# Performance work log

Measured on AMD Instinct MI355X. Metric: run time of the kernel, lower is better.

The kernel has to match this reference:

```python
import jax, jax.numpy as jnp
import numpy as np

N, CIN, PL, H, W, ETA, EXP = 8, 1024, 256, 64, 64, 8, 4
EPS = 1e-5

def _conv(x, w, stride=1, pad=0):
    return jax.lax.conv_general_dilated(
        x, w, (stride, stride), [(pad, pad), (pad, pad)],
        dimension_numbers=('NCHW', 'OIHW', 'NCHW'))

def _bn(x, p):
    # p: [4, C] = gamma, beta, running_mean, running_var (eval-mode BN)
    g, b, m, v = p[0], p[1], p[2], p[3]
    scale = (g / jnp.sqrt(v + EPS))[None, :, None, None]
    return (x - m[None, :, None, None]) * scale + b[None, :, None, None]

def _bn_params(key, c):
    k1, k2, k3, k4 = jax.random.split(key, 4)
    return jnp.stack([
        1.0 + 0.1 * jax.random.normal(k1, (c,)),
        0.1 * jax.random.normal(k2, (c,)),
        0.1 * jax.random.normal(k3, (c,)),
        jax.random.uniform(k4, (c,), minval=0.5, maxval=1.5)]).astype(jnp.float32)

def setup_inputs() -> dict:
    key = jax.random.key(0)
    ks = jax.random.split(key, 12)
    return {
        'x': jax.random.normal(ks[0], (N, CIN, H, W), jnp.float32),
        'norm_1': jnp.zeros((1, N + 1), jnp.float32),
        'norm_2': jnp.zeros((1, N + 1), jnp.float32),
        'flops': jnp.zeros((1, N + 1), jnp.float32),
        'ws_conv': 0.02 * jax.random.normal(ks[1], (1, CIN, 3, 3), jnp.float32),
        'ws_bias': jnp.zeros((1,), jnp.float32),
        'wc1': 0.02 * jax.random.normal(ks[2], (PL, CIN), jnp.float32),
        'bc1': jnp.zeros((PL,), jnp.float32),
        'wc2': 0.02 * jax.random.normal(ks[3], (PL, PL), jnp.float32),
        'bc2': jnp.zeros((PL,), jnp.float32),
        'w1': 0.05 * jax.random.normal(ks[4], (PL, CIN, 1, 1), jnp.float32),
        'bn1': _bn_params(ks[5], PL),
        'w2': 0.02 * jax.random.normal(ks[6], (PL, PL, 3, 3), jnp.float32),
        'bn2': _bn_params(ks[7], PL),
        'w3': 0.05 * jax.random.normal(ks[8], (PL * EXP, PL, 1, 1), jnp.float32),
        'bn3': _bn_params(ks[9], PL * EXP),
    }

def reference(x, norm_1, norm_2, flops, ws_conv, ws_bias, wc1, bc1, wc2, bc2,
              w1, bn1, w2, bn2, w3, bn3):
    n, c, h1, w1s = x.shape
    dt = x.dtype
    # ---- Mask_s: avg-pool by eta -> 3x3 conv to 1 ch -> hard gate (eval) ----
    pooled = x.reshape(n, c, h1 // ETA, ETA, w1s // ETA, ETA).mean((3, 5))
    logit_s = _conv(pooled, ws_conv, pad=1) + ws_bias[None, :, None, None]
    mask_s_m = (logit_s >= 0).astype(dt)            # [n,1,h/eta,w/eta]
    norm_s = mask_s_m.sum((1, 2, 3))                # [n]
    # ---- Mask_c1: GAP -> FC -> hard gate -> [n,PL,1,1] ----
    vec1 = x.mean((2, 3))                            # [n,CIN]
    mc1 = ((vec1 @ wc1.T + bc1) >= 0).astype(dt)[:, :, None, None]
    norm_c1 = mc1.sum((1, 2, 3))
    norm_c1_t = jnp.array([PL], dt)
    # ---- main path ----
    out = jax.nn.relu(_bn(_conv(x, w1), bn1))
    # nearest upsample of spatial mask back to (h1, w1)
    mask_s1 = jnp.repeat(jnp.repeat(mask_s_m, ETA, axis=2), ETA, axis=3)
    out = out * mc1 * mask_s1                        # eval-mode: both masks applied
    # ---- Mask_c2 on gated features ----
    vec2 = out.mean((2, 3))
    mc2 = ((vec2 @ wc2.T + bc2) >= 0).astype(dt)[:, :, None, None]
    norm_c2 = mc2.sum((1, 2, 3))
    norm_c2_t = jnp.array([PL], dt)
    out = jax.nn.relu(_bn(_conv(out, w2, pad=1), bn2))
    h2, w2s = out.shape[2], out.shape[3]
    mask_s2 = mask_s1                                # stride=1 -> same spatial size
    out = out * mc2 * mask_s2
    out = _bn(_conv(out, w3), bn3) * mask_s2
    out = jax.nn.relu(out + x)                       # identity (downsample=None)
    # ---- bookkeeping ----
    numel_s = jnp.array([mask_s_m[0].size], dt)      # 1 * h/eta * w/eta
    norm_1 = jnp.concatenate([norm_1, jnp.concatenate([norm_s, numel_s])[None]], 0)
    norm_2 = jnp.concatenate([norm_2, jnp.concatenate([norm_c1, norm_c1_t])[None]], 0)
    norm_2 = jnp.concatenate([norm_2, jnp.concatenate([norm_c2, norm_c2_t])[None]], 0)
    s_sum = mask_s2.sum((1, 2, 3))
    s_sum_1 = mask_s1.sum((1, 2, 3))
    fl = (s_sum_1 * norm_c1 * CIN
          + 9.0 * s_sum * norm_c2 * norm_c1
          + s_sum * (PL * EXP) * norm_c2)
    fl_full = jnp.array([h1 * w1s * PL * CIN
                         + 9 * h2 * w2s * PL * PL
                         + h2 * w2s * PL * PL * EXP], dt)
    flops = jnp.concatenate([flops, jnp.concatenate([fl, fl_full])[None]], 0)
    return out, norm_1, norm_2, flops
```

## Files before the change

### kernel.cpp

```cpp
#include <hip/hip_runtime.h>
#include <cstddef>
#include <cstdint>

#define NN   8
#define CIN  1024
#define PL   256
#define PE   1024
#define HW   4096
#define EPS_ 1e-5f

typedef _Float16 half8 __attribute__((ext_vector_type(8)));
typedef float floatx4 __attribute__((ext_vector_type(4)));

union HU { uint4 u4; half8 h8; };

__device__ inline uint32_t pack2(float v) {
  union { _Float16 f[2]; uint32_t u; } z;
  _Float16 h = (_Float16)v;
  z.f[0] = h;
  z.f[1] = (_Float16)(v - (float)h);
  return z.u;
}

static const size_t OFF1 = 33554432;
static const size_t OFF2 = OFF1 + 18;
static const size_t OFF3 = OFF2 + 27;

__global__ __launch_bounds__(256) void k_prep(
    const float* __restrict__ bn1, const float* __restrict__ bn2,
    const float* __restrict__ bn3, const float* __restrict__ w1,
    const float* __restrict__ w2, const float* __restrict__ w3,
    _Float16* __restrict__ w1f, _Float16* __restrict__ w2f,
    _Float16* __restrict__ w3f,
    float* __restrict__ s1, float* __restrict__ t1,
    float* __restrict__ s2, float* __restrict__ t2,
    float* __restrict__ s3, float* __restrict__ t3,
    float* __restrict__ pooled, float* __restrict__ vec2) {
  unsigned idx = blockIdx.x * 256 + threadIdx.x;
  if (idx < 262144u) {
    int p = idx >> 10, c = idx & 1023;
    float v = w1[idx]; _Float16 h = (_Float16)v;
    int lane = (((c & 31) >> 3) << 4) | (p & 15);
    size_t base = (size_t)(((c >> 5) * 16 + (p >> 4))) * 1024 + lane * 8 + (c & 7);
    w1f[base] = h; w1f[base + 512] = (_Float16)(v - (float)h);
  } else if (idx < 524288u) {
    unsigned i = idx - 262144u;
    int p = i >> 8, c = i & 255;
    float v = w3[i]; _Float16 h = (_Float16)v;
    int lane = (((c & 31) >> 3) << 4) | (p & 15);
    size_t base = (size_t)((c >> 5) * 64 + (p >> 4)) * 1024 + lane * 8 + (c & 7);
    w3f[base] = h; w3f[base + 512] = (_Float16)(v - (float)h);
  } else if (idx < 1114112u) {
    unsigned i = idx - 524288u;
    unsigned p = i / 2304u, rem = i - p * 2304u;
    unsigned c = rem / 9u, tap = rem - c * 9u;
    float v = w2[i]; _Float16 h = (_Float16)v;
    int lane = (((c & 31) >> 3) << 4) | (p & 15);
    size_t base = (size_t)((tap * 8 + (c >> 5)) * 16 + (p >> 4)) * 1024 + lane * 8 + (c & 7);
    w2f[base] = h; w2f[base + 512] = (_Float16)(v - (float)h);
  } else if (idx < 1638400u) {
    pooled[idx - 1114112u] = 0.f;
  } else if (idx < 1640448u) {
    vec2[idx - 1638400u] = 0.f;
  } else if (idx < 1641984u) {
    int i = idx - 1640448u;
    if (i < 256) {
      float g = bn1[i], b = bn1[256 + i], m = bn1[512 + i], v = bn1[768 + i];
      float s = g / sqrtf(v + EPS_);
      s1[i] = s; t1[i] = b - m * s;
    } else if (i < 512) {
      int c = i - 256;
      float g = bn2[c], b = bn2[256 + c], m = bn2[512 + c], v = bn2[768 + c];
      float s = g / sqrtf(v + EPS_);
      s2[c] = s; t2[c] = b - m * s;
    } else {
      int c = i - 512;
      float g = bn3[c], b = bn3[1024 + c], m = bn3[2048 + c], v = bn3[3072 + c];
      float s = g / sqrtf(v + EPS_);
      s3[c] = s; t3[c] = b - m * s;
    }
  }
}

__global__ __launch_bounds__(256) void k_xsplit(const float* __restrict__ x,
                                                _Float16* __restrict__ xh,
                                                _Float16* __restrict__ xl,
                                                float* __restrict__ pooled) {
  const int bx = blockIdx.x;
  const int hw0 = bx * 64, c0 = blockIdx.y * 64, n = blockIdx.z;
  const int t = threadIdx.x;
  __shared__ float Tt[64][65];
#pragma unroll
  for (int j = 0; j < 4; ++j) {
    int rc = (t >> 4) + j * 16;
    int col = (t & 15) * 4;
    float4 v = *(const float4*)(x + ((size_t)(n * 1024) + c0 + rc) * 4096 + hw0 + col);
    Tt[col + 0][rc] = v.x; Tt[col + 1][rc] = v.y;
    Tt[col + 2][rc] = v.z; Tt[col + 3][rc] = v.w;
  }
  __syncthreads();
  {
    const int ch = t & 63, grp = t >> 6;
    const int pr = bx >> 3;
#pragma unroll
    for (int cc = 0; cc < 2; ++cc) {
      int pc = grp * 2 + cc;
      float s = 0.f;
#pragma unroll
      for (int px = 0; px < 8; ++px) s += Tt[pc * 8 + px][ch];
      atomicAdd(&pooled[(size_t)(n * 64 + pr * 8 + pc) * 1024 + c0 + ch], s * (1.f / 64.f));
    }
  }
  const int hwl = t >> 2, part = t & 3;
  size_t ob = ((size_t)(n * 4096) + hw0 + hwl) * 1024 + c0 + part * 16;
#pragma unroll
  for (int k2 = 0; k2 < 2; ++k2) {
    half8 vh, vl;
#pragma unroll
    for (int e = 0; e < 8; ++e) {
      float v = Tt[hwl][part * 16 + k2 * 8 + e];
      _Float16 hh = (_Float16)v;
      vh[e] = hh; vl[e] = (_Float16)(v - (float)hh);
    }
    *(half8*)(xh + ob + k2 * 8) = vh;
    *(half8*)(xl + ob + k2 * 8) = vl;
  }
}

__global__ __launch_bounds__(256) void k_vec1(const float* __restrict__ pooled,
                                              float* __restrict__ vec1) {
  const int n = blockIdx.x, t = threadIdx.x;
#pragma unroll
  for (int j = 0; j < 4; ++j) {
    int c = j * 256 + t;
    float s = 0.f;
    for (int cell = 0; cell < 64; ++cell)
      s += pooled[(size_t)(n * 64 + cell) * 1024 + c];
    vec1[n * 1024 + c] = s * (1.f / 64.f);
  }
}

__global__ __launch_bounds__(256) void k_masks(const float* __restrict__ wsconv,
                                               const float* __restrict__ wsbias,
                                               const float* __restrict__ pooled,
                                               float* __restrict__ masks) {
  const int bid = blockIdx.x;
  const int n = bid >> 6, cell = bid & 63, ph = cell >> 3, pw = cell & 7;
  const int tid = threadIdx.x;
  const float* pl = pooled + (size_t)n * 64 * 1024;
  float acc = 0.f;
#pragma unroll
  for (int kh = 0; kh < 3; ++kh) {
    int py = ph + kh - 1;
    if (py < 0 || py > 7) continue;
#pragma unroll
    for (int kw = 0; kw < 3; ++kw) {
      int px = pw + kw - 1;
      if (px < 0 || px > 7) continue;
      float4 pv = *(const float4*)(pl + (size_t)(py * 8 + px) * 1024 + tid * 4);
      int k = kh * 3 + kw;
      acc += pv.x * wsconv[(tid * 4 + 0) * 9 + k] + pv.y * wsconv[(tid * 4 + 1) * 9 + k]
           + pv.z * wsconv[(tid * 4 + 2) * 9 + k] + pv.w * wsconv[(tid * 4 + 3) * 9 + k];
    }
  }
  __shared__ float red[256];
  red[tid] = acc;
  __syncthreads();
  for (int s = 128; s > 0; s >>= 1) {
    if (tid < s) red[tid] += red[tid + s];
    __syncthreads();
  }
  if (tid == 0) masks[n * 64 + cell] = (red[0] + wsbias[0] >= 0.f) ? 1.f : 0.f;
}

__global__ __launch_bounds__(64) void k_mc1(const float* __restrict__ wc1,
                                            const float* __restrict__ bc1,
                                            const float* __restrict__ vec1,
                                            float* __restrict__ mc1) {
  const int bx = blockIdx.x;
  const int n = bx >> 8, p = bx & 255;
  const int t = threadIdx.x;
  const float* v = vec1 + n * 1024;
  const float* wr = wc1 + (size_t)p * 1024;
  float acc = 0.f;
#pragma unroll
  for (int j = 0; j < 16; ++j) acc += v[t + 64 * j] * wr[t + 64 * j];
  for (int m = 1; m < 64; m <<= 1) acc += __shfl_xor(acc, m, 64);
  if (t == 0) mc1[n * 256 + p] = (acc + bc1[p] >= 0.f) ? 1.f : 0.f;
}

__global__ __launch_bounds__(256) void k_gemm1(
    const _Float16* __restrict__ xh, const _Float16* __restrict__ xl,
    const _Float16* __restrict__ w1f,
    const float* __restrict__ s1, const float* __restrict__ t1,
    const float* __restrict__ mc1, const float* __restrict__ masks,
    _Float16* __restrict__ o1h, _Float16* __restrict__ o1l) {
  const int hw0 = blockIdx.x * 128, p0 = blockIdx.y * 128, n = blockIdx.z;
  const int t = threadIdx.x;
  const int lane = t & 63, w = t >> 6;
  const int l15 = lane & 15, l4 = lane >> 4;
  const int wr = w >> 1, wc = w & 1;
  __shared__ __align__(16) char smem[33792];
  _Float16* LB = (_Float16*)smem;
  floatx4 acc[4][4] = {};
  const size_t nb = (size_t)(n * 4096) + hw0;
  const _Float16* wfp = w1f + (size_t)((p0 >> 4) + wr * 4) * 1024 + lane * 8;
  for (int kc = 0; kc < 32; ++kc) {
    const int c0 = kc * 32;
    half8 tmp[4];
#pragma unroll
    for (int j = 0; j < 4; ++j) {
      int u = t + 256 * j;
      int kind = u >> 9, rem = u & 511, row = rem >> 2, q = rem & 3;
      const _Float16* src = (kind ? xl : xh) + (nb + row) * 1024 + c0 + q * 8;
      tmp[j] = *(const half8*)src;
    }
    half8 ah[4], al[4];
#pragma unroll
    for (int i = 0; i < 4; ++i) {
      const _Float16* ap = wfp + (size_t)(kc * 16 + i) * 1024;
      ah[i] = *(const half8*)ap;
      al[i] = *(const half8*)(ap + 512);
    }
    __syncthreads();
#pragma unroll
    for (int j = 0; j < 4; ++j) {
      int u = t + 256 * j;
      int kind = u >> 9, rem = u & 511, row = rem >> 2, q = rem & 3;
      *(half8*)(LB + kind * 5120 + row * 40 + q * 8) = tmp[j];
    }
    __syncthreads();
    half8 bh[4], bl[4];
#pragma unroll
    for (int j = 0; j < 4; ++j) {
      int r = (wc * 64 + j * 16 + l15) * 40 + l4 * 8;
      bh[j] = *(const half8*)(LB + r);
      bl[j] = *(const half8*)(LB + 5120 + r);
    }
#pragma unroll
    for (int i = 0; i < 4; ++i)
#pragma unroll
      for (int j = 0; j < 4; ++j) {
        acc[i][j] = __builtin_amdgcn_mfma_f32_16x16x32_f16(ah[i], bh[j], acc[i][j], 0, 0, 0);
        acc[i][j] = __builtin_amdgcn_mfma_f32_16x16x32_f16(ah[i], bl[j], acc[i][j], 0, 0, 0);
        acc[i][j] = __builtin_amdgcn_mfma_f32_16x16x32_f16(al[i], bh[j], acc[i][j], 0, 0, 0);
      }
  }
  uint32_t (*T)[132] = (uint32_t(*)[132])smem;
  const int n64 = n * 64;
  const float* mc1n = mc1 + n * 256;
  for (int h = 0; h < 2; ++h) {
    __syncthreads();
    if (wc == h) {
#pragma unroll
      for (int j = 0; j < 4; ++j) {
        int nl = j * 16 + l15;
        int pix = hw0 + h * 64 + nl;
        float msk = masks[n64 + ((pix >> 9) << 3) + ((pix & 63) >> 3)];
#pragma unroll
        for (int i = 0; i < 4; ++i) {
          uint32_t pk[4];
#pragma unroll
          for (int r = 0; r < 4; ++r) {
            int m = wr * 64 + i * 16 + l4 * 4 + r;
            int p = p0 + m;
            float val = fmaxf(fmaf(acc[i][j][r], s1[p], t1[p]), 0.f) * (mc1n[p] * msk);
            pk[r] = pack2(val);
          }
          *(uint4*)&T[nl][wr * 64 + i * 16 + l4 * 4] = *(uint4*)pk;
        }
      }
    }
    __syncthreads();
    {
      int row = t >> 2, seg = t & 3;
      int pix = hw0 + h * 64 + row;
      _Float16* dh = o1h + ((size_t)(n * 4096) + pix) * 256 + p0 + seg * 32;
      _Float16* dl = o1l + ((size_t)(n * 4096) + pix) * 256 + p0 + seg * 32;
#pragma unroll
      for (int k2 = 0; k2 < 4; ++k2) {
        uint4 a = *(uint4*)&T[row][seg * 32 + k2 * 8];
        uint4 b = *(uint4*)&T[row][seg * 32 + k2 * 8 + 4];
        uint4 hv = make_uint4((a.x & 0xFFFFu) | (a.y << 16), (a.z & 0xFFFFu) | (a.w << 16),
                              (b.x & 0xFFFFu) | (b.y << 16), (b.z & 0xFFFFu) | (b.w << 16));
        uint4 lv = make_uint4((a.x >> 16) | (a.y & 0xFFFF0000u), (a.z >> 16) | (a.w & 0xFFFF0000u),
                              (b.x >> 16) | (b.y & 0xFFFF0000u), (b.z >> 16) | (b.w & 0xFFFF0000u));
        *(uint4*)(dh + k2 * 8) = hv;
        *(uint4*)(dl + k2 * 8) = lv;
      }
    }
  }
}

__global__ __launch_bounds__(256) void k_vec2(const _Float16* __restrict__ o1h,
                                              const _Float16* __restrict__ o1l,
                                              float* __restrict__ vec2) {
  const int n = blockIdx.x >> 5, ch = blockIdx.x & 31;
  const int t = threadIdx.x;
  const _Float16* bh = o1h + ((size_t)(n * 4096) + ch * 128) * 256 + t;
  const _Float16* bl = o1l + ((size_t)(n * 4096) + ch * 128) * 256 + t;
  float s = 0.f;
  for (int i = 0; i < 128; ++i)
    s += (float)bh[(size_t)i * 256] + (float)bl[(size_t)i * 256];
  atomicAdd(&vec2[n * 256 + t], s * (1.f / 4096.f));
}

__global__ __launch_bounds__(64) void k_mc2(const float* __restrict__ wc2,
                                            const float* __restrict__ bc2,
                                            const float* __restrict__ vec2,
                                            float* __restrict__ mc2) {
  const int bx = blockIdx.x;
  const int n = bx >> 8, p = bx & 255;
  const int t = threadIdx.x;
  const float* v = vec2 + n * 256;
  const float* wr = wc2 + (size_t)p * 256;
  float acc = 0.f;
#pragma unroll
  for (int j = 0; j < 4; ++j) acc += v[t + 64 * j] * wr[t + 64 * j];
  for (int m = 1; m < 64; m <<= 1) acc += __shfl_xor(acc, m, 64);
  if (t == 0) mc2[n * 256 + p] = (acc + bc2[p] >= 0.f) ? 1.f : 0.f;
}

__global__ __launch_bounds__(256) void k_gemm2(
    const _Float16* __restrict__ o1h, const _Float16* __restrict__ o1l,
    const _Float16* __restrict__ w2f,
    const float* __restrict__ s2, const float* __restrict__ t2,
    const float* __restrict__ mc2, const float* __restrict__ masks,
    _Float16* __restrict__ o2h, _Float16* __restrict__ o2l) {
  const int bt = blockIdx.x, p0 = blockIdx.y * 128, n = blockIdx.z;
  const int hw0 = bt * 128;
  const int t = threadIdx.x;
  const int lane = t & 63, w = t >> 6;
  const int l15 = lane & 15, l4 = lane >> 4;
  const int wr = w >> 1, wc = w & 1;
  __shared__ __align__(16) char smem[42240];
  _Float16* LB = (_Float16*)smem;
  floatx4 acc[4][4] = {};
  const size_t onb = (size_t)(n * 4096);
  const int row0 = bt * 2 - 1;
  const _Float16* wfp = w2f + (size_t)((p0 >> 4) + wr * 4) * 1024 + lane * 8;
  for (int kc = 0; kc < 8; ++kc) {
    const int c0 = kc * 32;
    HU st[9];
#pragma unroll
    for (int j2 = 0; j2 < 9; ++j2) {
      int u = t + 256 * j2;
      st[j2].u4 = make_uint4(0u, 0u, 0u, 0u);
      if (u < 2112) {
        int kind = (u >= 1056) ? 1 : 0;
        int rem = u - kind * 1056;
        int pix = rem >> 2, q = rem & 3;
        int sr = pix / 66, sc = pix - sr * 66;
        int gr = row0 + sr, gc = sc - 1;
        if (gr >= 0 && gr < 64 && gc >= 0 && gc < 64) {
          const _Float16* src = (kind ? o1l : o1h) + (onb + gr * 64 + gc) * 256 + c0 + q * 8;
          st[j2].h8 = *(const half8*)src;
        }
      }
    }
    __syncthreads();
#pragma unroll
    for (int j2 = 0; j2 < 9; ++j2) {
      int u = t + 256 * j2;
      if (u < 2112) {
        int kind = (u >= 1056) ? 1 : 0;
        int rem = u - kind * 1056;
        int pix = rem >> 2, q = rem & 3;
        *(half8*)(LB + kind * 10560 + pix * 40 + q * 8) = st[j2].h8;
      }
    }
    __syncthreads();
#pragma unroll 1
    for (int tap = 0; tap < 9; ++tap) {
      const int kh = tap / 3, kw = tap - kh * 3;
      half8 ah[4], al[4], bh[4], bl[4];
#pragma unroll
      for (int i = 0; i < 4; ++i) {
        const _Float16* ap = wfp + (size_t)(((tap * 8 + kc) * 16) + i) * 1024;
        ah[i] = *(const half8*)ap;
        al[i] = *(const half8*)(ap + 512);
      }
#pragma unroll
      for (int j = 0; j < 4; ++j) {
        int pi = (wc + kh) * 66 + j * 16 + l15 + kw;
        bh[j] = *(const half8*)(LB + pi * 40 + l4 * 8);
        bl[j] = *(const half8*)(LB + 10560 + pi * 40 + l4 * 8);
      }
#pragma unroll
      for (int i = 0; i < 4; ++i)
#pragma unroll
        for (int j = 0; j < 4; ++j) {
          acc[i][j] = __builtin_amdgcn_mfma_f32_16x16x32_f16(ah[i], bh[j], acc[i][j], 0, 0, 0);
          acc[i][j] = __builtin_amdgcn_mfma_f32_16x16x32_f16(ah[i], bl[j], acc[i][j], 0, 0, 0);
          acc[i][j] = __builtin_amdgcn_mfma_f32_16x16x32_f16(al[i], bh[j], acc[i][j], 0, 0, 0);
        }
    }
  }
  uint32_t (*T)[132] = (uint32_t(*)[132])smem;
  const int n64 = n * 64;
  const float* mc2n = mc2 + n * 256;
  for (int h = 0; h < 2; ++h) {
    __syncthreads();
    if (wc == h) {
#pragma unroll
      for (int j = 0; j < 4; ++j) {
        int nl = j * 16 + l15;
        int pix = hw0 + h * 64 + nl;
        float msk = masks[n64 + ((pix >> 9) << 3) + ((pix & 63) >> 3)];
#pragma unroll
        for (int i = 0; i < 4; ++i) {
          uint32_t pk[4];
#pragma unroll
          for (int r = 0; r < 4; ++r) {
            int m = wr * 64 + i * 16 + l4 * 4 + r;
            int p = p0 + m;
            float val = fmaxf(fmaf(acc[i][j][r], s2[p], t2[p]), 0.f) * (mc2n[p] * msk);
            pk[r] = pack2(val);
          }
          *(uint4*)&T[nl][wr * 64 + i * 16 + l4 * 4] = *(uint4*)pk;
        }
      }
    }
    __syncthreads();
    {
      int row = t >> 2, seg = t & 3;
      int pix = hw0 + h * 64 + row;
      _Float16* dh = o2h + ((size_t)(n * 4096) + pix) * 256 + p0 + seg * 32;
      _Float16* dl = o2l + ((size_t)(n * 4096) + pix) * 256 + p0 + seg * 32;
#pragma unroll
      for (int k2 = 0; k2 < 4; ++k2) {
        uint4 a = *(uint4*)&T[row][seg * 32 + k2 * 8];
        uint4 b = *(uint4*)&T[row][seg * 32 + k2 * 8 + 4];
        uint4 hv = make_uint4((a.x & 0xFFFFu) | (a.y << 16), (a.z & 0xFFFFu) | (a.w << 16),
                              (b.x & 0xFFFFu) | (b.y << 16), (b.z & 0xFFFFu) | (b.w << 16));
        uint4 lv = make_uint4((a.x >> 16) | (a.y & 0xFFFF0000u), (a.z >> 16) | (a.w & 0xFFFF0000u),
                              (b.x >> 16) | (b.y & 0xFFFF0000u), (b.z >> 16) | (b.w & 0xFFFF0000u));
        *(uint4*)(dh + k2 * 8) = hv;
        *(uint4*)(dl + k2 * 8) = lv;
      }
    }
  }
}

__global__ __launch_bounds__(256) void k_gemm3(
    const _Float16* __restrict__ o2h, const _Float16* __restrict__ o2l,
    const _Float16* __restrict__ w3f,
    const float* __restrict__ s3, const float* __restrict__ t3,
    const float* __restrict__ masks, const float* __restrict__ x,
    float* __restrict__ out) {
  const int hw0 = blockIdx.x * 128, p0 = blockIdx.y * 128, n = blockIdx.z;
  const int t = threadIdx.x;
  const int lane = t & 63, w = t >> 6;
  const int l15 = lane & 15, l4 = lane >> 4;
  const int wr = w >> 1, wc = w & 1;
  __shared__ __align__(16) char smem[20480];
  _Float16* LB = (_Float16*)smem;
  floatx4 acc[4][4] = {};
  const size_t nb = (size_t)(n * 4096) + hw0;
  const _Float16* wfp = w3f + (size_t)((p0 >> 4) + wr * 4) * 1024 + lane * 8;
  for (int kc = 0; kc < 8; ++kc) {
    const int c0 = kc * 32;
    half8 tmp[4];
#pragma unroll
    for (int j = 0; j < 4; ++j) {
      int u = t + 256 * j;
      int kind = u >> 9, rem = u & 511, row = rem >> 2, q = rem & 3;
      const _Float16* src = (kind ? o2l : o2h) + (nb + row) * 256 + c0 + q * 8;
      tmp[j] = *(const half8*)src;
    }
    half8 ah[4], al[4];
#pragma unroll
    for (int i = 0; i < 4; ++i) {
      const _Float16* ap = wfp + (size_t)(kc * 64 + i) * 1024;
      ah[i] = *(const half8*)ap;
      al[i] = *(const half8*)(ap + 512);
    }
    __syncthreads();
#pragma unroll
    for (int j = 0; j < 4; ++j) {
      int u = t + 256 * j;
      int kind = u >> 9, rem = u & 511, row = rem >> 2, q = rem & 3;
      *(half8*)(LB + kind * 5120 + row * 40 + q * 8) = tmp[j];
    }
    __syncthreads();
    half8 bh[4], bl[4];
#pragma unroll
    for (int j = 0; j < 4; ++j) {
      int r = (wc * 64 + j * 16 + l15) * 40 + l4 * 8;
      bh[j] = *(const half8*)(LB + r);
      bl[j] = *(const half8*)(LB + 5120 + r);
    }
#pragma unroll
    for (int i = 0; i < 4; ++i)
#pragma unroll
      for (int j = 0; j < 4; ++j) {
        acc[i][j] = __builtin_amdgcn_mfma_f32_16x16x32_f16(ah[i], bh[j], acc[i][j], 0, 0, 0);
        acc[i][j] = __builtin_amdgcn_mfma_f32_16x16x32_f16(ah[i], bl[j], acc[i][j], 0, 0, 0);
        acc[i][j] = __builtin_amdgcn_mfma_f32_16x16x32_f16(al[i], bh[j], acc[i][j], 0, 0, 0);
      }
    __syncthreads();
  }
  const int n64 = n * 64;
  float msk[4];
#pragma unroll
  for (int j = 0; j < 4; ++j) {
    int pix = hw0 + wc * 64 + j * 16 + l15;
    msk[j] = masks[n64 + ((pix >> 9) << 3) + ((pix & 63) >> 3)];
  }
#pragma unroll
  for (int i = 0; i < 4; ++i)
#pragma unroll
    for (int r = 0; r < 4; ++r) {
      int m = wr * 64 + i * 16 + l4 * 4 + r;
      int pe = p0 + m;
      float sc = s3[pe], sh = t3[pe];
      size_t rowoff = ((size_t)(n * 1024) + pe) * 4096 + hw0;
#pragma unroll
      for (int j = 0; j < 4; ++j) {
        int nl = wc * 64 + j * 16 + l15;
        float val = fmaf(acc[i][j][r], sc, sh) * msk[j];
        size_t off = rowoff + nl;
        out[off] = fmaxf(val + x[off], 0.f);
      }
    }
}

__global__ __launch_bounds__(64) void k_book(const float* __restrict__ n1in,
                                             const float* __restrict__ n2in,
                                             const float* __restrict__ flin,
                                             const float* __restrict__ masks,
                                             const float* __restrict__ mc1,
                                             const float* __restrict__ mc2,
                                             float* __restrict__ out) {
  const int t = threadIdx.x;
  if (t < 9) {
    out[OFF1 + t] = n1in[t];
    out[OFF2 + t] = n2in[t];
    out[OFF3 + t] = flin[t];
  }
  if (t < 8) {
    float ns = 0.f, nc1 = 0.f, nc2 = 0.f;
    for (int i = 0; i < 64; ++i) ns += masks[t * 64 + i];
    for (int i = 0; i < 256; ++i) nc1 += mc1[t * 256 + i];
    for (int i = 0; i < 256; ++i) nc2 += mc2[t * 256 + i];
    out[OFF1 + 9 + t] = ns;
    out[OFF2 + 9 + t] = nc1;
    out[OFF2 + 18 + t] = nc2;
    const float s = ns * 64.f;
    const float term1 = (s * nc1) * 1024.f;
    const float term2 = ((9.f * s) * nc2) * nc1;
    const float term3 = (s * 1024.f) * nc2;
    out[OFF3 + 9 + t] = (term1 + term2) + term3;
  }
  if (t == 9) {
    out[OFF1 + 17] = 64.f;
    out[OFF2 + 17] = 256.f;
    out[OFF2 + 26] = 256.f;
    out[OFF3 + 17] = 4563402752.f;
  }
}

extern "C" void kernel_launch(void* const* d_in, const int* in_sizes, int n_in,
                              void* d_out, int out_size, void* d_ws, size_t ws_size,
                              hipStream_t stream) {
  (void)in_sizes; (void)n_in; (void)out_size; (void)ws_size;
  const float* x      = (const float*)d_in[0];
  const float* n1in   = (const float*)d_in[1];
  const float* n2in   = (const float*)d_in[2];
  const float* flin   = (const float*)d_in[3];
  const float* wsconv = (const float*)d_in[4];
  const float* wsbias = (const float*)d_in[5];
  const float* wc1    = (const float*)d_in[6];
  const float* bc1    = (const float*)d_in[7];
  const float* wc2    = (const float*)d_in[8];
  const float* bc2    = (const float*)d_in[9];
  const float* w1     = (const float*)d_in[10];
  const float* bn1    = (const float*)d_in[11];
  const float* w2     = (const float*)d_in[12];
  const float* bn2    = (const float*)d_in[13];
  const float* w3     = (const float*)d_in[14];
  const float* bn3    = (const float*)d_in[15];
  float* out = (float*)d_out;

  _Float16* xh = (_Float16*)d_out;
  _Float16* xl = xh + 33554432;

  char* W = (char*)d_ws;
  _Float16* o1h = (_Float16*)(W);
  _Float16* o1l = (_Float16*)(W + 16777216);
  _Float16* o2h = (_Float16*)(W + 33554432);
  _Float16* o2l = (_Float16*)(W + 50331648);
  _Float16* w1f = (_Float16*)(W + 67108864);
  _Float16* w2f = (_Float16*)(W + 68157440);
  _Float16* w3f = (_Float16*)(W + 70516736);
  float* pooled = (float*)(W + 71565312);
  float* vec1   = (float*)(W + 73662464);
  float* vec2   = (float*)(W + 73695232);
  float* masksP = (float*)(W + 73703424);
  float* mc1    = (float*)(W + 73705472);
  float* mc2    = (float*)(W + 73713664);
  float* s1     = (float*)(W + 73721856);
  float* t1     = (float*)(W + 73722880);
  float* s2     = (float*)(W + 73723904);
  float* t2     = (float*)(W + 73724928);
  float* s3     = (float*)(W + 73725952);
  float* t3     = (float*)(W + 73730048);

  hipLaunchKernelGGL(k_prep, dim3(6414), dim3(256), 0, stream,
                     bn1, bn2, bn3, w1, w2, w3, w1f, w2f, w3f,
                     s1, t1, s2, t2, s3, t3, pooled, vec2);
  hipLaunchKernelGGL(k_xsplit, dim3(64, 16, NN), dim3(256), 0, stream, x, xh, xl, pooled);
  hipLaunchKernelGGL(k_vec1, dim3(NN), dim3(256), 0, stream, pooled, vec1);
  hipLaunchKernelGGL(k_masks, dim3(NN * 64), dim3(256), 0, stream, wsconv, wsbias, pooled, masksP);
  hipLaunchKernelGGL(k_mc1, dim3(NN * PL), dim3(64), 0, stream, wc1, bc1, vec1, mc1);
  hipLaunchKernelGGL(k_gemm1, dim3(32, 2, NN), dim3(256), 0, stream,
                     xh, xl, w1f, s1, t1, mc1, masksP, o1h, o1l);
  hipLaunchKernelGGL(k_vec2, dim3(NN * 32), dim3(256), 0, stream, o1h, o1l, vec2);
  hipLaunchKernelGGL(k_mc2, dim3(NN * PL), dim3(64), 0, stream, wc2, bc2, vec2, mc2);
  hipLaunchKernelGGL(k_gemm2, dim3(32, 2, NN), dim3(256), 0, stream,
                     o1h, o1l, w2f, s2, t2, mc2, masksP, o2h, o2l);
  hipLaunchKernelGGL(k_gemm3, dim3(32, 8, NN), dim3(256), 0, stream,
                     o2h, o2l, w3f, s3, t3, masksP, x, out);
  hipLaunchKernelGGL(k_book, dim3(1), dim3(64), 0, stream,
                     n1in, n2in, flin, masksP, mc1, mc2, out);
}
```

Measured before the change: 747.3 us.

## Software-pipeline global loads in the three GEMM kernels via register prefetch

Each GEMM kernel now prefetches the next K-chunk's activation tile and weight fragments into registers while the MFMAs for the current chunk run. In gemm2 the next channel strip is loaded during the nine-tap loop, and the weight fragments are prefetched one tap ahead. The goal is to hide global-memory latency behind the matrix math. The kernels also gain launch_bounds(256,2), which raises register pressure alongside the extra prefetch registers and risks spills or lower occupancy.

```diff
diff --git a/kernel.cpp b/kernel.cpp
--- a/kernel.cpp
+++ b/kernel.cpp
@@ -189,7 +189,7 @@
   if (t == 0) mc1[n * 256 + p] = (acc + bc1[p] >= 0.f) ? 1.f : 0.f;
 }
 
-__global__ __launch_bounds__(256) void k_gemm1(
+__global__ __launch_bounds__(256, 2) void k_gemm1(
     const _Float16* __restrict__ xh, const _Float16* __restrict__ xl,
     const _Float16* __restrict__ w1f,
     const float* __restrict__ s1, const float* __restrict__ t1,
@@ -205,31 +205,51 @@
   floatx4 acc[4][4] = {};
   const size_t nb = (size_t)(n * 4096) + hw0;
   const _Float16* wfp = w1f + (size_t)((p0 >> 4) + wr * 4) * 1024 + lane * 8;
+  const int uk = t >> 9 ? 1 : 0;
+  const int urow = (t & 511) >> 2, uq = t & 3;
+
+  half8 tmpP[4], ahP[4], alP[4];
+#pragma unroll
+  for (int j = 0; j < 4; ++j) {
+    int u = t + 256 * j;
+    int kind = u >> 9, rem = u & 511, row = rem >> 2, q = rem & 3;
+    tmpP[j] = *(const half8*)((kind ? xl : xh) + (nb + row) * 1024 + q * 8);
+  }
+#pragma unroll
+  for (int i = 0; i < 4; ++i) {
+    const _Float16* ap = wfp + (size_t)i * 1024;
+    ahP[i] = *(const half8*)ap;
+    alP[i] = *(const half8*)(ap + 512);
+  }
+  (void)uk; (void)urow; (void)uq;
+#pragma unroll 1
   for (int kc = 0; kc < 32; ++kc) {
-    const int c0 = kc * 32;
-    half8 tmp[4];
+    __syncthreads();
 #pragma unroll
     for (int j = 0; j < 4; ++j) {
       int u = t + 256 * j;
       int kind = u >> 9, rem = u & 511, row = rem >> 2, q = rem & 3;
-      const _Float16* src = (kind ? xl : xh) + (nb + row) * 1024 + c0 + q * 8;
-      tmp[j] = *(const half8*)src;
-    }
+      *(half8*)(LB + kind * 5120 + row * 40 + q * 8) = tmpP[j];
+    }
+    __syncthreads();
     half8 ah[4], al[4];
 #pragma unroll
-    for (int i = 0; i < 4; ++i) {
-      const _Float16* ap = wfp + (size_t)(kc * 16 + i) * 1024;
-      ah[i] = *(const half8*)ap;
-      al[i] = *(const half8*)(ap + 512);
-    }
-    __syncthreads();
-#pragma unroll
-    for (int j = 0; j < 4; ++j) {
-      int u = t + 256 * j;
-      int kind = u >> 9, rem = u & 511, row = rem >> 2, q = rem & 3;
-      *(half8*)(LB + kind * 5120 + row * 40 + q * 8) = tmp[j];
-    }
-    __syncthreads();
+    for (int i = 0; i < 4; ++i) { ah[i] = ahP[i]; al[i] = alP[i]; }
+    if (kc < 31) {
+      const int c1 = (kc + 1) * 32;
+#pragma unroll
+      for (int j = 0; j < 4; ++j) {
+        int u = t + 256 * j;
+        int kind = u >> 9, rem = u & 511, row = rem >> 2, q = rem & 3;
+        tmpP[j] = *(const half8*)((kind ? xl : xh) + (nb + row) * 1024 + c1 + q * 8);
+      }
+#pragma unroll
+      for (int i = 0; i < 4; ++i) {
+        const _Float16* ap = wfp + (size_t)((kc + 1) * 16 + i) * 1024;
+        ahP[i] = *(const half8*)ap;
+        alP[i] = *(const half8*)(ap + 512);
+      }
+    }
     half8 bh[4], bl[4];
 #pragma unroll
     for (int j = 0; j < 4; ++j) {
@@ -321,7 +341,7 @@
   if (t == 0) mc2[n * 256 + p] = (acc + bc2[p] >= 0.f) ? 1.f : 0.f;
 }
 
-__global__ __launch_bounds__(256) void k_gemm2(
+__global__ __launch_bounds__(256, 2) void k_gemm2(
     const _Float16* __restrict__ o1h, const _Float16* __restrict__ o1l,
     const _Float16* __restrict__ w2f,
     const float* __restrict__ s2, const float* __restrict__ t2,
@@ -339,9 +359,12 @@
   const size_t onb = (size_t)(n * 4096);
   const int row0 = bt * 2 - 1;
   const _Float16* wfp = w2f + (size_t)((p0 >> 4) + wr * 4) * 1024 + lane * 8;
-  for (int kc = 0; kc < 8; ++kc) {
+
+  HU st[9];
+  half8 ahP[4], alP[4];
+
+  auto load_strip = [&](int kc) {
     const int c0 = kc * 32;
-    HU st[9];
 #pragma unroll
     for (int j2 = 0; j2 < 9; ++j2) {
       int u = t + 256 * j2;
@@ -358,7 +381,8 @@
         }
       }
     }
-    __syncthreads();
+  };
+  auto write_strip = [&]() {
 #pragma unroll
     for (int j2 = 0; j2 < 9; ++j2) {
       int u = t + 256 * j2;
@@ -369,17 +393,32 @@
         *(half8*)(LB + kind * 10560 + pix * 40 + q * 8) = st[j2].h8;
       }
     }
-    __syncthreads();
+  };
+  auto loadA = [&](int tap, int kc) {
+#pragma unroll
+    for (int i = 0; i < 4; ++i) {
+      const _Float16* ap = wfp + (size_t)(((tap * 8 + kc) * 16) + i) * 1024;
+      ahP[i] = *(const half8*)ap;
+      alP[i] = *(const half8*)(ap + 512);
+    }
+  };
+
+  load_strip(0);
+  write_strip();
+  loadA(0, 0);
+  __syncthreads();
 #pragma unroll 1
+  for (int kc = 0; kc < 8; ++kc) {
+    if (kc < 7) load_strip(kc + 1);
+#pragma unroll
     for (int tap = 0; tap < 9; ++tap) {
+      half8 ah[4], al[4];
+#pragma unroll
+      for (int i = 0; i < 4; ++i) { ah[i] = ahP[i]; al[i] = alP[i]; }
+      if (tap < 8) loadA(tap + 1, kc);
+      else if (kc < 7) loadA(0, kc + 1);
       const int kh = tap / 3, kw = tap - kh * 3;
-      half8 ah[4], al[4], bh[4], bl[4];
-#pragma unroll
-      for (int i = 0; i < 4; ++i) {
-        const _Float16* ap = wfp + (size_t)(((tap * 8 + kc) * 16) + i) * 1024;
-        ah[i] = *(const half8*)ap;
-        al[i] = *(const half8*)(ap + 512);
-      }
+      half8 bh[4], bl[4];
 #pragma unroll
       for (int j = 0; j < 4; ++j) {
         int pi = (wc + kh) * 66 + j * 16 + l15 + kw;
@@ -394,6 +433,11 @@
           acc[i][j] = __builtin_amdgcn_mfma_f32_16x16x32_f16(ah[i], bl[j], acc[i][j], 0, 0, 0);
           acc[i][j] = __builtin_amdgcn_mfma_f32_16x16x32_f16(al[i], bh[j], acc[i][j], 0, 0, 0);
         }
+    }
+    if (kc < 7) {
+      __syncthreads();
+      write_strip();
+      __syncthreads();
     }
   }
   uint32_t (*T)[132] = (uint32_t(*)[132])smem;
@@ -442,7 +486,7 @@
   }
 }
 
-__global__ __launch_bounds__(256) void k_gemm3(
+__global__ __launch_bounds__(256, 2) void k_gemm3(
     const _Float16* __restrict__ o2h, const _Float16* __restrict__ o2l,
     const _Float16* __restrict__ w3f,
     const float* __restrict__ s3, const float* __restrict__ t3,
@@ -458,31 +502,48 @@
   floatx4 acc[4][4] = {};
   const size_t nb = (size_t)(n * 4096) + hw0;
   const _Float16* wfp = w3f + (size_t)((p0 >> 4) + wr * 4) * 1024 + lane * 8;
+
+  half8 tmpP[4], ahP[4], alP[4];
+#pragma unroll
+  for (int j = 0; j < 4; ++j) {
+    int u = t + 256 * j;
+    int kind = u >> 9, rem = u & 511, row = rem >> 2, q = rem & 3;
+    tmpP[j] = *(const half8*)((kind ? o2l : o2h) + (nb + row) * 256 + q * 8);
+  }
+#pragma unroll
+  for (int i = 0; i < 4; ++i) {
+    const _Float16* ap = wfp + (size_t)i * 1024;
+    ahP[i] = *(const half8*)ap;
+    alP[i] = *(const half8*)(ap + 512);
+  }
+#pragma unroll 1
   for (int kc = 0; kc < 8; ++kc) {
-    const int c0 = kc * 32;
-    half8 tmp[4];
+    __syncthreads();
 #pragma unroll
     for (int j = 0; j < 4; ++j) {
       int u = t + 256 * j;
       int kind = u >> 9, rem = u & 511, row = rem >> 2, q = rem & 3;
-      const _Float16* src = (kind ? o2l : o2h) + (nb + row) * 256 + c0 + q * 8;
-      tmp[j] = *(const half8*)src;
-    }
+      *(half8*)(LB + kind * 5120 + row * 40 + q * 8) = tmpP[j];
+    }
+    __syncthreads();
     half8 ah[4], al[4];
 #pragma unroll
-    for (int i = 0; i < 4; ++i) {
-      const _Float16* ap = wfp + (size_t)(kc * 64 + i) * 1024;
-      ah[i] = *(const half8*)ap;
-      al[i] = *(const half8*)(ap + 512);
-    }
-    __syncthreads();
-#pragma unroll
-    for (int j = 0; j < 4; ++j) {
-      int u = t + 256 * j;
-      int kind = u >> 9, rem = u & 511, row = rem >> 2, q = rem & 3;
-      *(half8*)(LB + kind * 5120 + row * 40 + q * 8) = tmp[j];
-    }
-    __syncthreads();
+    for (int i = 0; i < 4; ++i) { ah[i] = ahP[i]; al[i] = alP[i]; }
+    if (kc < 7) {
+      const int c1 = (kc + 1) * 32;
+#pragma unroll
+      for (int j = 0; j < 4; ++j) {
+        int u = t + 256 * j;
+        int kind = u >> 9, rem = u & 511, row = rem >> 2, q = rem & 3;
+        tmpP[j] = *(const half8*)((kind ? o2l : o2h) + (nb + row) * 256 + c1 + q * 8);
+      }
+#pragma unroll
+      for (int i = 0; i < 4; ++i) {
+        const _Float16* ap = wfp + (size_t)((kc + 1) * 64 + i) * 1024;
+        ahP[i] = *(const half8*)ap;
+        alP[i] = *(const half8*)(ap + 512);
+      }
+    }
     half8 bh[4], bl[4];
 #pragma unroll
     for (int j = 0; j < 4; ++j) {
@@ -498,7 +559,6 @@
         acc[i][j] = __builtin_amdgcn_mfma_f32_16x16x32_f16(ah[i], bl[j], acc[i][j], 0, 0, 0);
         acc[i][j] = __builtin_amdgcn_mfma_f32_16x16x32_f16(al[i], bh[j], acc[i][j], 0, 0, 0);
       }
-    __syncthreads();
   }
   const int n64 = n * 64;
   float msk[4];
```

New measurement: 600.3 us. 1.24x faster.
